# Kernel tuning notes

Measured on AMD Instinct MI355X. Metric: run time of the kernel, lower is better.

The kernel has to match this reference:

```python
import jax, jax.numpy as jnp
import numpy as np
import math

B, S, D = 4, 2048, 1024
TAU = 0.5

def setup_inputs() -> dict:
    key = jax.random.key(0)
    ks = jax.random.split(key, 10)
    s = 1.0 / math.sqrt(D)
    return {
        "node_emb": jax.random.normal(ks[0], (B, S, D), jnp.float32),
        "label_emb": jax.random.normal(ks[1], (B, S, D), jnp.float32),
        "Wq": jax.random.uniform(ks[2], (D, D), jnp.float32, -s, s),
        "bq": jax.random.uniform(ks[3], (D,), jnp.float32, -s, s),
        "Wk": jax.random.uniform(ks[4], (D, D), jnp.float32, -s, s),
        "bk": jax.random.uniform(ks[5], (D,), jnp.float32, -s, s),
        "Wv": jax.random.uniform(ks[6], (D, D), jnp.float32, -s, s),
        "bv": jax.random.uniform(ks[7], (D,), jnp.float32, -s, s),
        "Wp": jax.random.uniform(ks[8], (D, D), jnp.float32, -s, s),
        "bp": jax.random.uniform(ks[9], (D,), jnp.float32, -s, s),
    }

def reference(node_emb, label_emb, Wq, bq, Wk, bk, Wv, bv, Wp, bp):
    # Q from label_emb; K, V from node_emb (torch Linear: x @ W.T + b)
    Q = label_emb @ Wq.T + bq          # [B, S, D]
    K = node_emb @ Wk.T + bk           # [B, S, D]
    V = node_emb @ Wv.T + bv           # [B, S, D]
    d = node_emb.shape[-1]
    score = jnp.einsum('bqd,bkd->bqk', Q, K) / jnp.sqrt(jnp.float32(d))
    # causal (lower-triangular) mask, masked_fill(-1e9) BEFORE the tau scale
    causal = jnp.tril(jnp.ones((score.shape[-2], score.shape[-1]), bool))
    score = jnp.where(causal[None, :, :], score, jnp.float32(-1e9))
    attn = jax.nn.softmax(score * TAU, axis=-1)  # [B, S, S]
    # proj_drop is Dropout(0.1); reference runs in eval mode (identity)
    z = jnp.einsum('bqk,bkd->bqd', attn, V)
    return z @ Wp.T + bp
```

## Files before the change

kernel.cpp:

```cpp
#include <hip/hip_runtime.h>
#include <hip/hip_bf16.h>
#include <stdint.h>

using bf16 = __hip_bfloat16;
typedef __bf16 bf16x8 __attribute__((ext_vector_type(8)));
typedef float f32x4 __attribute__((ext_vector_type(4)));
typedef unsigned short u16x8 __attribute__((ext_vector_type(8)));
typedef unsigned short u16x4 __attribute__((ext_vector_type(4)));

#define AS1 __attribute__((address_space(1)))
#define AS3 __attribute__((address_space(3)))

__device__ inline unsigned short f2b(float f) {
    union { __hip_bfloat16 h; unsigned short u; } cv;
    cv.h = __float2bfloat16(f);
    return cv.u;
}

__global__ __launch_bounds__(256) void cvt_pair(const float* __restrict__ a, const float* __restrict__ b,
                                                u16x8* __restrict__ oa, u16x8* __restrict__ ob, long n8) {
    const float* in = blockIdx.y ? b : a;
    u16x8* out = blockIdx.y ? ob : oa;
    long i = (long)blockIdx.x * blockDim.x + threadIdx.x;
    const long stride = (long)gridDim.x * blockDim.x;
    const float4* in4 = (const float4*)in;
    for (; i < n8; i += stride) {
        float4 x = in4[2 * i], y = in4[2 * i + 1];
        u16x8 o;
        o[0] = f2b(x.x); o[1] = f2b(x.y); o[2] = f2b(x.z); o[3] = f2b(x.w);
        o[4] = f2b(y.x); o[5] = f2b(y.y); o[6] = f2b(y.z); o[7] = f2b(y.w);
        out[i] = o;
    }
}

__global__ __launch_bounds__(256) void cvt_quad(const float* __restrict__ a, const float* __restrict__ b,
                                                const float* __restrict__ c, const float* __restrict__ d,
                                                u16x8* __restrict__ oa, u16x8* __restrict__ ob,
                                                u16x8* __restrict__ oc, u16x8* __restrict__ od, long n8) {
    const int y = blockIdx.y;
    const float* in = y == 0 ? a : (y == 1 ? b : (y == 2 ? c : d));
    u16x8* out = y == 0 ? oa : (y == 1 ? ob : (y == 2 ? oc : od));
    long i = (long)blockIdx.x * blockDim.x + threadIdx.x;
    const long stride = (long)gridDim.x * blockDim.x;
    const float4* in4 = (const float4*)in;
    for (; i < n8; i += stride) {
        float4 x = in4[2 * i], z = in4[2 * i + 1];
        u16x8 o;
        o[0] = f2b(x.x); o[1] = f2b(x.y); o[2] = f2b(x.z); o[3] = f2b(x.w);
        o[4] = f2b(z.x); o[5] = f2b(z.y); o[6] = f2b(z.z); o[7] = f2b(z.w);
        out[i] = o;
    }
}

template <typename T> __device__ inline void storev(T* p, float v);
template <> __device__ inline void storev<float>(float* p, float v) { *p = v; }
template <> __device__ inline void storev<bf16>(bf16* p, float v) { *p = __float2bfloat16(v); }

template <typename OutT, int MODE, int BN>
__global__ __launch_bounds__(512, 2) void gemmX(
    const bf16* __restrict__ A0, const bf16* __restrict__ A1,
    const bf16* __restrict__ B0p, const bf16* __restrict__ B1p,
    OutT* __restrict__ C0, OutT* __restrict__ C1,
    const float* __restrict__ bias0, const float* __restrict__ bias1,
    float scale, int lda, int ldb, int ldc, int Kdim,
    long sA, long sB, long sC)
{
    constexpr int LDSZ = (BN == 256) ? 131072 : 98304;
    constexpr int BUFS = (BN == 256) ? 65536 : 49152;
    __shared__ __align__(16) char lds[LDSZ];

    const int nwg = gridDim.x;
    const int bid = blockIdx.x;
    const int s = (nwg & 7) ? bid : ((bid & 7) * (nwg >> 3) + (bid >> 3));

    int bm, ccol0, rowB0, seg = 0;
    const bf16 *A, *B;
    OutT* C;
    const float* bias = nullptr;

    if constexpr (MODE == 0) {
        bm = s >> 3; const int bnl = s & 7; seg = bnl >> 2;
        A = A0; B = B0p; rowB0 = bnl * 256;
        C = seg ? C1 : C0; bias = seg ? bias1 : bias0;
        ccol0 = (bnl & 3) * 256;
    } else if constexpr (MODE == 1) {
        seg = s >> 7; const int r = s & 127; bm = r >> 2; const int bn = r & 3;
        A = seg ? A1 : A0; B = seg ? B1p : B0p;
        C = seg ? C1 : C0; bias = seg ? nullptr : bias0;
        rowB0 = bn * 256; ccol0 = bn * 256;
    } else if constexpr (MODE == 2) {
        const int z = s / 36, f = s % 36;
        int m = 0;
        while ((m + 1) * (m + 2) / 2 <= f) ++m;
        bm = m; const int bn = f - m * (m + 1) / 2;
        A = A0 + (long)z * sA; B = B0p + (long)z * sB; C = C0 + (long)z * sC;
        rowB0 = bn * 256; ccol0 = bn * 256;
    } else {
        const int z = s >> 6, r = s & 63; bm = r >> 3; const int bn = r & 7;
        A = A0 + (long)z * sA; B = B0p + (long)z * sB; C = C0 + (long)z * sC;
        rowB0 = bn * 128; ccol0 = bn * 128; bias = bias0;
    }

    int KT = Kdim >> 6;
    if constexpr (MODE == 3) { const int lim = 4 * (bm + 1); if (lim < KT) KT = lim; }
    const int NIT = KT >> 1;

    const int tid = threadIdx.x;
    const int lane = tid & 63;
    const int w = tid >> 6;
    constexpr int WR = (BN == 256) ? 128 : 64;
    const int wm = (BN == 256) ? (w >> 2) : (w >> 1);
    const int wn = (BN == 256) ? (w & 3) : (w & 1);

    const int rowA0 = bm * 256;

    const int rr  = tid >> 3;
    const int lch = (tid & 7) ^ (rr & 7);
    const bf16* gAt = A + (long)(rowA0 + rr) * lda + lch * 8;
    const bf16* gBt = B + (long)(rowB0 + rr) * ldb + lch * 8;

#define LA(b) (lds + (b) * BUFS)
#define LB(b) (lds + 32768 + (b) * BUFS)

    auto SG2 = [&](const bf16* g, int ld, char* dst) {
        __builtin_amdgcn_global_load_lds((const AS1 void*)g,
            (AS3 void*)(dst + tid * 16), 16, 0, 0);
        __builtin_amdgcn_global_load_lds((const AS1 void*)(g + (long)64 * ld),
            (AS3 void*)(dst + 8192 + tid * 16), 16, 0, 0);
    };
    auto ST_A = [&](int kt, int half, int b) {
        SG2(gAt + (long)kt * 64 + (long)half * 128 * lda, lda, LA(b) + half * 16384);
    };
    auto ST_B = [&](int kt, int half, int b) {
        SG2(gBt + (long)kt * 64 + (long)half * 128 * ldb, ldb, LB(b) + half * 16384);
    };
    auto ST_B1 = [&](int kt, int b) {
        SG2(gBt + (long)kt * 64, ldb, LB(b));
    };

    const int abase = (wm * WR + (lane & 15)) * 128;
    const int bbase = (wn * 64 + (lane & 15)) * 128;
    const int cc0 = (((lane >> 4) << 4)) ^ ((lane & 7) << 4);
    const int cc1 = cc0 ^ 64;

#define RAF(b, mh, mi, kk) (*(const bf16x8*)(LA(b) + abase + (mh)*8192 + (mi)*2048 + ((kk) ? cc1 : cc0)))
#define RBF(b, ni, kk)     (*(const bf16x8*)(LB(b) + bbase + (ni)*2048 + ((kk) ? cc1 : cc0)))

    f32x4 acc[(BN == 256) ? 8 : 4][4] = {};
    bf16x8 ar[4][2], blo[2][2], bhi[2][2];

#define RD_A2(b, mh, MI0) { ar[MI0][0] = RAF(b, mh, MI0, 0); ar[MI0][1] = RAF(b, mh, MI0, 1); \
                            ar[(MI0)+1][0] = RAF(b, mh, (MI0)+1, 0); ar[(MI0)+1][1] = RAF(b, mh, (MI0)+1, 1); }
#define RD_BLO(b)   { blo[0][0] = RBF(b, 0, 0); blo[0][1] = RBF(b, 0, 1); blo[1][0] = RBF(b, 1, 0); blo[1][1] = RBF(b, 1, 1); }
#define RD_BHI(b)   { bhi[0][0] = RBF(b, 2, 0); bhi[0][1] = RBF(b, 2, 1); bhi[1][0] = RBF(b, 3, 0); bhi[1][1] = RBF(b, 3, 1); }

#define MQ1(MI, bb, MH, NB) { \
    f32x4 t0_ = acc[(MH)*4 + (MI)][(NB)]; \
    t0_ = __builtin_amdgcn_mfma_f32_16x16x32_bf16(ar[MI][0], bb[0][0], t0_, 0, 0, 0); \
    t0_ = __builtin_amdgcn_mfma_f32_16x16x32_bf16(ar[MI][1], bb[0][1], t0_, 0, 0, 0); \
    acc[(MH)*4 + (MI)][(NB)] = t0_; \
    f32x4 t1_ = acc[(MH)*4 + (MI)][(NB) + 1]; \
    t1_ = __builtin_amdgcn_mfma_f32_16x16x32_bf16(ar[MI][0], bb[1][0], t1_, 0, 0, 0); \
    t1_ = __builtin_amdgcn_mfma_f32_16x16x32_bf16(ar[MI][1], bb[1][1], t1_, 0, 0, 0); \
    acc[(MH)*4 + (MI)][(NB) + 1] = t1_; }

#define WAIT_LGKM0 { asm volatile("s_waitcnt lgkmcnt(0)" ::: "memory"); __builtin_amdgcn_sched_barrier(0); }
#define WAIT_LGKM4 { asm volatile("s_waitcnt lgkmcnt(4)" ::: "memory"); __builtin_amdgcn_sched_barrier(0); }
#define SCHEDB     __builtin_amdgcn_sched_barrier(0)

    auto BAR = [&]() { __builtin_amdgcn_s_barrier(); SCHEDB; };
    auto PRIO1 = [&]() { __builtin_amdgcn_s_setprio(1); };
    auto PRIO0 = [&]() { __builtin_amdgcn_s_setprio(0); };

    if constexpr (BN == 256) {
        ST_A(0, 0, 0); ST_A(0, 1, 0); ST_B(0, 0, 0); ST_B(0, 1, 0);
        ST_B(1, 0, 1); ST_B(1, 1, 1);
        asm volatile("s_waitcnt vmcnt(4)" ::: "memory");
        BAR();

        for (int i = 0; i < NIT; ++i) {
            const int t0 = 2 * i;
            const bool last = (i == NIT - 1);

            RD_BLO(0); RD_A2(0, 0, 0); SCHEDB; RD_A2(0, 0, 2);
            ST_A(t0 + 1, 0, 1);
            BAR(); WAIT_LGKM4; PRIO1();
            MQ1(0, blo, 0, 0); MQ1(1, blo, 0, 0);
            WAIT_LGKM0;
            MQ1(2, blo, 0, 0); MQ1(3, blo, 0, 0);
            PRIO0(); BAR();
            RD_BHI(0);
            ST_A(t0 + 1, 1, 1);
            BAR(); WAIT_LGKM0; PRIO1();
            MQ1(0, bhi, 0, 2); MQ1(1, bhi, 0, 2); MQ1(2, bhi, 0, 2); MQ1(3, bhi, 0, 2);
            PRIO0(); BAR();
            RD_A2(0, 1, 0); SCHEDB; RD_A2(0, 1, 2);
            if (!last) ST_B(t0 + 2, 0, 0);
            BAR(); WAIT_LGKM4; PRIO1();
            MQ1(0, bhi, 1, 2); MQ1(1, bhi, 1, 2);
            WAIT_LGKM0;
            MQ1(2, bhi, 1, 2); MQ1(3, bhi, 1, 2);
            PRIO0(); BAR();
            if (!last) { ST_B(t0 + 2, 1, 0);
                         asm volatile("s_waitcnt vmcnt(4)" ::: "memory"); }
            else       { asm volatile("s_waitcnt vmcnt(0)" ::: "memory"); }
            BAR(); WAIT_LGKM0; PRIO1();
            MQ1(0, blo, 1, 0); MQ1(1, blo, 1, 0); MQ1(2, blo, 1, 0); MQ1(3, blo, 1, 0);
            PRIO0(); BAR();
            RD_BLO(1); RD_A2(1, 0, 0); SCHEDB; RD_A2(1, 0, 2);
            if (!last) ST_A(t0 + 2, 0, 0);
            BAR(); WAIT_LGKM4; PRIO1();
            MQ1(0, blo, 0, 0); MQ1(1, blo, 0, 0);
            WAIT_LGKM0;
            MQ1(2, blo, 0, 0); MQ1(3, blo, 0, 0);
            PRIO0(); BAR();
            RD_BHI(1);
            if (!last) ST_A(t0 + 2, 1, 0);
            BAR(); WAIT_LGKM0; PRIO1();
            MQ1(0, bhi, 0, 2); MQ1(1, bhi, 0, 2); MQ1(2, bhi, 0, 2); MQ1(3, bhi, 0, 2);
            PRIO0(); BAR();
            RD_A2(1, 1, 0); SCHEDB; RD_A2(1, 1, 2);
            if (!last) ST_B(t0 + 3, 0, 1);
            BAR(); WAIT_LGKM4; PRIO1();
            MQ1(0, bhi, 1, 2); MQ1(1, bhi, 1, 2);
            WAIT_LGKM0;
            MQ1(2, bhi, 1, 2); MQ1(3, bhi, 1, 2);
            PRIO0(); BAR();
            if (!last) { ST_B(t0 + 3, 1, 1);
                         asm volatile("s_waitcnt vmcnt(4)" ::: "memory"); }
            BAR(); WAIT_LGKM0; PRIO1();
            MQ1(0, blo, 1, 0); MQ1(1, blo, 1, 0); MQ1(2, blo, 1, 0); MQ1(3, blo, 1, 0);
            PRIO0(); BAR();
        }
    } else {
        ST_A(0, 0, 0); ST_A(0, 1, 0); ST_B1(0, 0);
        ST_A(1, 0, 1); ST_A(1, 1, 1); ST_B1(1, 1);
        asm volatile("s_waitcnt vmcnt(6)" ::: "memory");
        BAR();

        for (int i = 0; i < NIT; ++i) {
            const int t0 = 2 * i;
            const bool last = (i == NIT - 1);

            RD_BLO(0); RD_A2(0, 0, 0); RD_A2(0, 0, 2); SCHEDB; RD_BHI(0);
            BAR(); WAIT_LGKM4; PRIO1();
            MQ1(0, blo, 0, 0); MQ1(1, blo, 0, 0); MQ1(2, blo, 0, 0); MQ1(3, blo, 0, 0);
            PRIO0(); BAR();

            if (!last) { ST_A(t0 + 2, 0, 0); ST_A(t0 + 2, 1, 0);
                         asm volatile("s_waitcnt vmcnt(4)" ::: "memory"); }
            else       { asm volatile("s_waitcnt vmcnt(0)" ::: "memory"); }
            BAR(); WAIT_LGKM0; PRIO1();
            MQ1(0, bhi, 0, 2); MQ1(1, bhi, 0, 2); MQ1(2, bhi, 0, 2); MQ1(3, bhi, 0, 2);
            PRIO0(); BAR();

            RD_BLO(1); RD_A2(1, 0, 0); RD_A2(1, 0, 2); SCHEDB; RD_BHI(1);
            if (!last) ST_B1(t0 + 2, 0);
            BAR(); WAIT_LGKM4; PRIO1();
            MQ1(0, blo, 0, 0); MQ1(1, blo, 0, 0); MQ1(2, blo, 0, 0); MQ1(3, blo, 0, 0);
            PRIO0(); BAR();

            if (!last) { ST_A(t0 + 3, 0, 1); ST_A(t0 + 3, 1, 1); ST_B1(t0 + 3, 1);
                         asm volatile("s_waitcnt vmcnt(6)" ::: "memory"); }
            BAR(); WAIT_LGKM0; PRIO1();
            MQ1(0, bhi, 0, 2); MQ1(1, bhi, 0, 2); MQ1(2, bhi, 0, 2); MQ1(3, bhi, 0, 2);
            PRIO0(); BAR();
        }
    }

    if constexpr (BN == 256) {
        char* tw = lds + w * 16384;
        if (MODE == 1 && seg == 1) {
#pragma unroll
            for (int ni = 0; ni < 4; ++ni) {
                const int cl = ni * 16 + (lane & 15);
                const int sw = 8 * (cl & 7);
#pragma unroll
                for (int mi = 0; mi < 8; ++mi) {
                    const int rlb = mi * 16 + ((lane >> 4) << 2);
                    u16x4 o;
                    o[0] = f2b(acc[mi][ni][0]); o[1] = f2b(acc[mi][ni][1]);
                    o[2] = f2b(acc[mi][ni][2]); o[3] = f2b(acc[mi][ni][3]);
                    *(u16x4*)(tw + cl * 256 + 2 * (rlb ^ sw)) = o;
                }
            }
            asm volatile("s_waitcnt lgkmcnt(0)" ::: "memory");
            __builtin_amdgcn_sched_barrier(0);
            const int m0 = rowA0 + wm * 128;
            const int z2 = m0 >> 11, mr = m0 & 2047;
            bf16* CT = (bf16*)C + (long)z2 * 2097152 + (long)(ccol0 + wn * 64 + lane) * 2048 + mr;
            const char* tr = tw + lane * 256;
            const int sw2 = lane & 7;
#pragma unroll
            for (int rb = 0; rb < 16; ++rb) {
                u16x8 v = *(const u16x8*)(tr + 16 * (rb ^ sw2));
                *(u16x8*)(CT + 8 * rb) = v;
            }
        } else {
            const int q = lane >> 4, t = lane & 15;
            const int c0 = ccol0 + wn * 64 + t;
#pragma unroll
            for (int mi = 0; mi < 8; ++mi) {
                char* tm = tw + mi * 2048;
#pragma unroll
                for (int ni = 0; ni < 4; ++ni) {
                    const float bv = bias ? bias[c0 + ni * 16] : 0.0f;
                    const int cb = (t + 16 * ni) * 2;
#pragma unroll
                    for (int j = 0; j < 4; ++j) {
                        const int rl = q * 4 + j;
                        *(bf16*)(tm + rl * 128 + (cb ^ ((rl & 7) << 4))) =
                            __float2bfloat16(acc[mi][ni][j] * scale + bv);
                    }
                }
            }
            asm volatile("s_waitcnt lgkmcnt(0)" ::: "memory");
            __builtin_amdgcn_sched_barrier(0);
            const int rr2 = lane >> 2, chb = (lane & 3) * 2;
            const int gr0 = rowA0 + wm * 128;
            bf16* Cb = (bf16*)C;
            const int gcb = ccol0 + wn * 64;
#pragma unroll
            for (int mi = 0; mi < 8; ++mi) {
                const char* tm = tw + mi * 2048;
                const long gr = gr0 + mi * 16 + rr2;
#pragma unroll
                for (int k = 0; k < 2; ++k) {
                    const int chunk = chb + k;
                    u16x8 v = *(const u16x8*)(tm + rr2 * 128 + ((chunk << 4) ^ ((rr2 & 7) << 4)));
                    *(u16x8*)(Cb + gr * (long)ldc + gcb + chunk * 8) = v;
                }
            }
        }
    } else {
        const int r0 = rowA0 + wm * WR + ((lane >> 4) << 2);
        const int c0 = ccol0 + wn * 64 + (lane & 15);
        const bool HB = (bias != nullptr);
#pragma unroll
        for (int ni = 0; ni < 4; ++ni) {
            const int c = c0 + ni * 16;
            const float bv = HB ? bias[c] : 0.0f;
#pragma unroll
            for (int mi = 0; mi < 4; ++mi) {
#pragma unroll
                for (int j = 0; j < 4; ++j) {
                    const long r = r0 + mi * 16 + j;
                    storev<OutT>(&C[r * (long)ldc + c], acc[mi][ni][j] * scale + bv);
                }
            }
        }
    }
#undef RAF
#undef RBF
#undef RD_A2
#undef RD_BLO
#undef RD_BHI
#undef MQ1
#undef LA
#undef LB
}

__global__ __launch_bounds__(256) void softmax_causal(bf16* __restrict__ SP, int S) {
    const int i = blockIdx.x;
    bf16* row = SP + ((long)blockIdx.y * S + i) * (long)S;
    const int L = i + 1;
    const int tid = threadIdx.x;
    const int lane = tid & 63, wid = tid >> 6;

    float v[8];
    int nv = 0;
    float m = -3.0e38f;
    for (int j = tid; j < L; j += 256) {
        float x = __bfloat162float(row[j]);
        v[nv++] = x;
        m = fmaxf(m, x);
    }
#pragma unroll
    for (int d = 32; d; d >>= 1) m = fmaxf(m, __shfl_xor(m, d));
    __shared__ float redm[4], reds[4];
    if (lane == 0) redm[wid] = m;
    __syncthreads();
    m = fmaxf(fmaxf(redm[0], redm[1]), fmaxf(redm[2], redm[3]));

    float ssum = 0.f;
    for (int t = 0; t < nv; ++t) { v[t] = __expf(v[t] - m); ssum += v[t]; }
#pragma unroll
    for (int d = 32; d; d >>= 1) ssum += __shfl_xor(ssum, d);
    if (lane == 0) reds[wid] = ssum;
    __syncthreads();
    ssum = reds[0] + reds[1] + reds[2] + reds[3];
    const float inv = 1.0f / ssum;

    nv = 0;
    for (int j = tid; j < L; j += 256) row[j] = __float2bfloat16(v[nv++] * inv);
    const int Lpad = ((i >> 8) + 1) << 8;
    for (int j = L + tid; j < Lpad; j += 256) row[j] = __float2bfloat16(0.0f);
}

extern "C" void kernel_launch(void* const* d_in, const int* in_sizes, int n_in,
                              void* d_out, int out_size, void* d_ws, size_t ws_size,
                              hipStream_t stream) {
    const int B = 4, S = 2048, D = 1024;
    const long MD = (long)B * S * D;
    const float scale = 0.5f / 32.0f;

    const float* node  = (const float*)d_in[0];
    const float* label = (const float*)d_in[1];
    const float* Wq = (const float*)d_in[2];
    const float* bq = (const float*)d_in[3];
    const float* Wk = (const float*)d_in[4];
    const float* bk = (const float*)d_in[5];
    const float* Wv = (const float*)d_in[6];
    const float* bv = (const float*)d_in[7];
    const float* Wp = (const float*)d_in[8];
    const float* bp = (const float*)d_in[9];
    float* out = (float*)d_out;

    char* ws = (char*)d_ws;
    bf16* nodeb  = (bf16*)(ws);
    bf16* VTb    = nodeb;
    bf16* labelb = (bf16*)(ws + 16777216);
    bf16* Wqb = (bf16*)(ws + 33554432);
    bf16* Wkb = (bf16*)(ws + 35651584);
    bf16* Wvb = (bf16*)(ws + 37748736);
    bf16* Wpb = (bf16*)(ws + 39845888);
    bf16* Qb  = (bf16*)(ws + 41943040);
    bf16* Kb  = (bf16*)(ws + 58720256);
    bf16* Vb  = (bf16*)(ws + 75497472);
    bf16* SP  = (bf16*)(ws + 92274688);
    if (ws_size < 125829120UL) return;

    dim3 blk(256);

    cvt_pair<<<dim3(512, 2), blk, 0, stream>>>(node, label, (u16x8*)nodeb, (u16x8*)labelb, MD / 8);
    cvt_quad<<<dim3(64, 4), blk, 0, stream>>>(Wq, Wk, Wv, Wp,
        (u16x8*)Wqb, (u16x8*)Wkb, (u16x8*)Wvb, (u16x8*)Wpb, (long)D * D / 8);

    gemmX<bf16, 0, 256><<<256, 512, 0, stream>>>(
        nodeb, nullptr, Wkb, nullptr, Kb, Vb, bk, bv,
        1.0f, D, D, D, D, 0, 0, 0);

    gemmX<bf16, 1, 256><<<256, 512, 0, stream>>>(
        labelb, Vb, Wqb, Wpb, Qb, VTb, bq, nullptr,
        1.0f, D, D, D, D, 0, 0, 0);

    gemmX<bf16, 2, 256><<<144, 512, 0, stream>>>(
        Qb, nullptr, Kb, nullptr, SP, nullptr, nullptr, nullptr,
        scale, D, D, S, D, (long)S * D, (long)S * D, (long)S * S);

    softmax_causal<<<dim3(S, B), blk, 0, stream>>>(SP, S);

    gemmX<float, 3, 128><<<256, 512, 0, stream>>>(
        SP, nullptr, VTb, nullptr, out, nullptr, bp, nullptr,
        1.0f, S, S, D, S, (long)S * S, (long)D * S, (long)S * D);
}
```

Before: 188.2 us.

## Software-pipeline LDS fragment reads behind MFMA phases in BN=256 GEMM loop

Restructures the BN=256 main loop so LDS reads for the next MFMA phase are issued right after, or interleaved with, the current phase's MFMAs instead of before a barrier. Each phase now starts with a single lgkmcnt(0) wait plus barrier instead of two barriers, and the first phase's reads are hoisted into a prologue. The aim is to hide LDS latency under matrix work and cut barrier count. The risk is more register pressure and possible LDS read/write hazards if the buffer indexing does not line up with the new barrier placement.

```diff
diff --git a/kernel.cpp b/kernel.cpp
--- a/kernel.cpp
+++ b/kernel.cpp
@@ -167,6 +167,8 @@
 #define WAIT_LGKM0 { asm volatile("s_waitcnt lgkmcnt(0)" ::: "memory"); __builtin_amdgcn_sched_barrier(0); }
 #define WAIT_LGKM4 { asm volatile("s_waitcnt lgkmcnt(4)" ::: "memory"); __builtin_amdgcn_sched_barrier(0); }
 #define SCHEDB     __builtin_amdgcn_sched_barrier(0)
+#define PRE_SYNC { asm volatile("s_waitcnt lgkmcnt(0)" ::: "memory"); __builtin_amdgcn_sched_barrier(0); \
+                   __builtin_amdgcn_s_barrier(); __builtin_amdgcn_sched_barrier(0); }
 
     auto BAR = [&]() { __builtin_amdgcn_s_barrier(); SCHEDB; };
     auto PRIO1 = [&]() { __builtin_amdgcn_s_setprio(1); };
@@ -177,60 +179,60 @@
         ST_B(1, 0, 1); ST_B(1, 1, 1);
         asm volatile("s_waitcnt vmcnt(4)" ::: "memory");
         BAR();
+        RD_BLO(0); RD_A2(0, 0, 0); RD_A2(0, 0, 2);
 
         for (int i = 0; i < NIT; ++i) {
             const int t0 = 2 * i;
             const bool last = (i == NIT - 1);
 
-            RD_BLO(0); RD_A2(0, 0, 0); SCHEDB; RD_A2(0, 0, 2);
             ST_A(t0 + 1, 0, 1);
-            BAR(); WAIT_LGKM4; PRIO1();
-            MQ1(0, blo, 0, 0); MQ1(1, blo, 0, 0);
-            WAIT_LGKM0;
-            MQ1(2, blo, 0, 0); MQ1(3, blo, 0, 0);
-            PRIO0(); BAR();
+            PRE_SYNC; PRIO1();
             RD_BHI(0);
+            MQ1(0, blo, 0, 0); MQ1(1, blo, 0, 0); MQ1(2, blo, 0, 0); MQ1(3, blo, 0, 0);
+            PRIO0();
+
             ST_A(t0 + 1, 1, 1);
-            BAR(); WAIT_LGKM0; PRIO1();
+            PRE_SYNC; PRIO1();
             MQ1(0, bhi, 0, 2); MQ1(1, bhi, 0, 2); MQ1(2, bhi, 0, 2); MQ1(3, bhi, 0, 2);
-            PRIO0(); BAR();
-            RD_A2(0, 1, 0); SCHEDB; RD_A2(0, 1, 2);
+            RD_A2(0, 1, 0); RD_A2(0, 1, 2);
+            PRIO0();
+
             if (!last) ST_B(t0 + 2, 0, 0);
-            BAR(); WAIT_LGKM4; PRIO1();
-            MQ1(0, bhi, 1, 2); MQ1(1, bhi, 1, 2);
-            WAIT_LGKM0;
-            MQ1(2, bhi, 1, 2); MQ1(3, bhi, 1, 2);
-            PRIO0(); BAR();
+            PRE_SYNC; PRIO1();
+            MQ1(0, bhi, 1, 2); MQ1(1, bhi, 1, 2); MQ1(2, bhi, 1, 2); MQ1(3, bhi, 1, 2);
+            PRIO0();
+
             if (!last) { ST_B(t0 + 2, 1, 0);
                          asm volatile("s_waitcnt vmcnt(4)" ::: "memory"); }
             else       { asm volatile("s_waitcnt vmcnt(0)" ::: "memory"); }
-            BAR(); WAIT_LGKM0; PRIO1();
+            PRE_SYNC; PRIO1();
             MQ1(0, blo, 1, 0); MQ1(1, blo, 1, 0); MQ1(2, blo, 1, 0); MQ1(3, blo, 1, 0);
-            PRIO0(); BAR();
-            RD_BLO(1); RD_A2(1, 0, 0); SCHEDB; RD_A2(1, 0, 2);
+            RD_BLO(1); RD_A2(1, 0, 0); RD_A2(1, 0, 2);
+            PRIO0();
+
             if (!last) ST_A(t0 + 2, 0, 0);
-            BAR(); WAIT_LGKM4; PRIO1();
-            MQ1(0, blo, 0, 0); MQ1(1, blo, 0, 0);
-            WAIT_LGKM0;
-            MQ1(2, blo, 0, 0); MQ1(3, blo, 0, 0);
-            PRIO0(); BAR();
+            PRE_SYNC; PRIO1();
             RD_BHI(1);
+            MQ1(0, blo, 0, 0); MQ1(1, blo, 0, 0); MQ1(2, blo, 0, 0); MQ1(3, blo, 0, 0);
+            PRIO0();
+
             if (!last) ST_A(t0 + 2, 1, 0);
-            BAR(); WAIT_LGKM0; PRIO1();
+            PRE_SYNC; PRIO1();
             MQ1(0, bhi, 0, 2); MQ1(1, bhi, 0, 2); MQ1(2, bhi, 0, 2); MQ1(3, bhi, 0, 2);
-            PRIO0(); BAR();
-            RD_A2(1, 1, 0); SCHEDB; RD_A2(1, 1, 2);
+            RD_A2(1, 1, 0); RD_A2(1, 1, 2);
+            PRIO0();
+
             if (!last) ST_B(t0 + 3, 0, 1);
-            BAR(); WAIT_LGKM4; PRIO1();
-            MQ1(0, bhi, 1, 2); MQ1(1, bhi, 1, 2);
-            WAIT_LGKM0;
-            MQ1(2, bhi, 1, 2); MQ1(3, bhi, 1, 2);
-            PRIO0(); BAR();
+            PRE_SYNC; PRIO1();
+            MQ1(0, bhi, 1, 2); MQ1(1, bhi, 1, 2); MQ1(2, bhi, 1, 2); MQ1(3, bhi, 1, 2);
+            PRIO0();
+
             if (!last) { ST_B(t0 + 3, 1, 1);
                          asm volatile("s_waitcnt vmcnt(4)" ::: "memory"); }
-            BAR(); WAIT_LGKM0; PRIO1();
+            PRE_SYNC; PRIO1();
             MQ1(0, blo, 1, 0); MQ1(1, blo, 1, 0); MQ1(2, blo, 1, 0); MQ1(3, blo, 1, 0);
-            PRIO0(); BAR();
+            if (!last) { RD_BLO(0); RD_A2(0, 0, 0); RD_A2(0, 0, 2); }
+            PRIO0();
         }
     } else {
         ST_A(0, 0, 0); ST_A(0, 1, 0); ST_B1(0, 0);
```

Measured after the change: 182.9 us. -2.8%, faster.
